# Kernel tuning notes

Measured on AMD Instinct MI355X. Metric: run time of the kernel, lower is better.

## Reference

```python
import jax, jax.numpy as jnp
import numpy as np
import math

B, T, C, H = 4, 4096, 1024, 16
D = C // H

def setup_inputs() -> dict:
    key = jax.random.key(0)
    k1, k2, k3, k4, k5 = jax.random.split(key, 5)
    s = 1.0 / math.sqrt(C)
    return {
        "x": jax.random.normal(k1, (B, T, C), dtype=jnp.float32),
        "W_qkv": jax.random.normal(k2, (C, 3 * C), dtype=jnp.float32) * s,
        "b_qkv": jax.random.normal(k3, (3 * C,), dtype=jnp.float32) * 0.01,
        "W_out": jax.random.normal(k4, (C, C), dtype=jnp.float32) * s,
        "b_out": jax.random.normal(k5, (C,), dtype=jnp.float32) * 0.01,
    }

def reference(x, W_qkv, b_qkv, W_out, b_out):
    qkv = x @ W_qkv + b_qkv                      # (B,T,3C)
    q, k, v = jnp.split(qkv, 3, axis=2)
    q = q.reshape(B, T, H, D)
    k = k.reshape(B, T, H, D)
    v = v.reshape(B, T, H, D)
    # attention over the HEAD axis per (B,T): scores (B,T,H,H)
    att = jnp.einsum('bthd,btgd->bthg', q, k) / math.sqrt(D)
    att = jax.nn.softmax(att, axis=-1)
    out = jnp.einsum('bthg,btgd->bthd', att, v)  # (B,T,H,D)
    out = out.reshape(B, T, C)
    return out @ W_out + b_out
```

## Files before the change

kernel.cpp:

```cpp
#include <hip/hip_runtime.h>
#include <cstdint>
#include <cstddef>

constexpr int Bc = 4;
constexpr int Tc = 4096;
constexpr int Cc = 1024;
constexpr int Hc = 16;
constexpr int Dc = 64;
constexpr int Mc = Bc * Tc;
constexpr int N1c = 3 * Cc;
constexpr int Kc = Cc;
constexpr int KBc = Kc / 32;

typedef __bf16 bf16x8 __attribute__((ext_vector_type(8)));
typedef float  f32x4  __attribute__((ext_vector_type(4)));
typedef __attribute__((address_space(1))) uint32_t gu32;
typedef __attribute__((address_space(3))) uint32_t lu32;

__device__ __forceinline__ float bf2f(unsigned short u) {
    return __uint_as_float(((unsigned)u) << 16);
}
__device__ __forceinline__ unsigned short f2bf(float f) {
    unsigned u = __float_as_uint(f);
    u += 0x7FFF + ((u >> 16) & 1);
    return (unsigned short)(u >> 16);
}

__device__ __forceinline__ void load_lds16(const void* g, void* l) {
    __builtin_amdgcn_global_load_lds((gu32*)(uintptr_t)g, (lu32*)(uintptr_t)l, 16, 0, 0);
}


__global__ void convert_x_packed(const float* __restrict__ x,
                                 unsigned short* __restrict__ Ap) {
    const int w = threadIdx.x >> 6, lane = threadIdx.x & 63;
    const int t = blockIdx.x * 4 + w;
    const int mb = t >> 5, kb = t & 31;
    const int r = lane >> 2, c = lane & 3;
    const float* src = x + (size_t)(mb * 16 + r) * Kc + kb * 32 + c * 8;
    float4 f0 = *(const float4*)src;
    float4 f1 = *(const float4*)(src + 4);
    unsigned short u[8];
    u[0] = f2bf(f0.x); u[1] = f2bf(f0.y); u[2] = f2bf(f0.z); u[3] = f2bf(f0.w);
    u[4] = f2bf(f1.x); u[5] = f2bf(f1.y); u[6] = f2bf(f1.z); u[7] = f2bf(f1.w);
    *(uint4*)(Ap + (size_t)t * 512 + (c * 16 + r) * 8) = *(uint4*)u;
}

__global__ void transpose_convert_packed(const float* __restrict__ W,
                                         unsigned short* __restrict__ Bp,
                                         int K, int N) {
    __shared__ float tile[32][33];
    const int tx = threadIdx.x, ty = threadIdx.y;
    const int n0 = blockIdx.x * 32, k0 = blockIdx.y * 32;
    for (int i = ty; i < 32; i += 8)
        tile[i][tx] = W[(size_t)(k0 + i) * N + n0 + tx];
    __syncthreads();
    const int t = ty * 32 + tx;
    const int h = t >> 7, rr = t & 127, lane = rr >> 1, half = rr & 1;
    const int fq = lane >> 4, fn = lane & 15;
    unsigned short u[4];
    #pragma unroll
    for (int j = 0; j < 4; ++j)
        u[j] = f2bf(tile[fq * 8 + half * 4 + j][h * 16 + fn]);
    size_t tileIdx = (size_t)((n0 >> 4) + h) * (K >> 5) + (k0 >> 5);
    *(uint2*)(Bp + tileIdx * 512 + lane * 8 + half * 4) = *(uint2*)u;
}

template <bool OUT_BF16>
__global__ __launch_bounds__(256, 4) void lds_gemm_kernel(
    const unsigned short* __restrict__ Ap,
    const unsigned short* __restrict__ Bp,
    const float* __restrict__ bias,
    void* __restrict__ Cout,
    int M, int N, int K, int NB) {
    __shared__ unsigned short sA[16 * 512];
    __shared__ unsigned short sB[16 * 512];
    const int KB = K >> 5;
    const int MB = M >> 7;
    const int id   = blockIdx.x;
    const int xcd  = id & 7;
    const int per  = id >> 3;
    const int MSTR = MB >> 3;
    const int byl  = per & 7;
    const int bx   = (per >> 3) % NB;
    const int pass = per / (8 * NB);
    const int by   = xcd * MSTR + pass * 8 + byl;

    const int w    = threadIdx.x >> 6;
    const int lane = threadIdx.x & 63;
    const int m0 = by * 128;
    const int n0 = bx * 128;
    const int wm = (w >> 1) * 64;
    const int wn = (w & 1) * 64;

    const unsigned short* gA[4];
    const unsigned short* gB[4];
    unsigned short* lA[4];
    unsigned short* lB[4];
    #pragma unroll
    for (int i = 0; i < 4; ++i) {
        const int t  = w * 4 + i;
        const int mt = t >> 1, s = t & 1;
        gA[i] = Ap + ((size_t)(by * 8 + mt) * KB + s) * 512 + lane * 8;
        gB[i] = Bp + ((size_t)(bx * 8 + mt) * KB + s) * 512 + lane * 8;
        lA[i] = sA + t * 512;
        lB[i] = sB + t * 512;
    }

    const unsigned short* aP = sA + (wm >> 4) * 2 * 512 + lane * 8;
    const unsigned short* bP = sB + (wn >> 4) * 2 * 512 + lane * 8;

    const f32x4 zero4 = {0.f, 0.f, 0.f, 0.f};
    f32x4 acc[4][4];
    #pragma unroll
    for (int i = 0; i < 4; ++i)
        #pragma unroll
        for (int j = 0; j < 4; ++j) acc[i][j] = zero4;

    const int NIT = K >> 6;
    #pragma unroll 1
    for (int jt = 0; jt < NIT; ++jt) {
        #pragma unroll
        for (int i = 0; i < 4; ++i) {
            load_lds16(gA[i], lA[i]);
            load_lds16(gB[i], lB[i]);
        }
        #pragma unroll
        for (int i = 0; i < 4; ++i) { gA[i] += 1024; gB[i] += 1024; }
        __syncthreads();

        #pragma unroll
        for (int kk = 0; kk < 2; ++kk) {
            bf16x8 af[4], bfr[4];
            #pragma unroll
            for (int mi = 0; mi < 4; ++mi)
                af[mi]  = *(const bf16x8*)(aP + (mi * 2 + kk) * 512);
            #pragma unroll
            for (int ni = 0; ni < 4; ++ni)
                bfr[ni] = *(const bf16x8*)(bP + (ni * 2 + kk) * 512);
            #pragma unroll
            for (int mi = 0; mi < 4; ++mi)
                #pragma unroll
                for (int ni = 0; ni < 4; ++ni)
                    acc[mi][ni] = __builtin_amdgcn_mfma_f32_16x16x32_bf16(
                        af[mi], bfr[ni], acc[mi][ni], 0, 0, 0);
        }
        __syncthreads();
    }

    const int fr = lane & 15;
    const int fq = lane >> 4;
    #pragma unroll
    for (int mi = 0; mi < 4; ++mi) {
        #pragma unroll
        for (int ni = 0; ni < 4; ++ni) {
            int row = m0 + wm + mi * 16 + fq * 4;
            int col = n0 + wn + ni * 16 + fr;
            float bb = bias[col];
            #pragma unroll
            for (int r = 0; r < 4; ++r) {
                float v = acc[mi][ni][r] + bb;
                if (OUT_BF16)
                    ((unsigned short*)Cout)[(size_t)(row + r) * N + col] = f2bf(v);
                else
                    ((float*)Cout)[(size_t)(row + r) * N + col] = v;
            }
        }
    }
}

__global__ __launch_bounds__(256) void attn_mfma_kernel(
    const unsigned short* __restrict__ qkv,
    unsigned short* __restrict__ attP) {
    __shared__ char smem[4 * 3584];
    const int w    = threadIdx.x >> 6;
    const int lane = threadIdx.x & 63;
    const int m    = lane & 15;
    const int q    = lane >> 4;
    const int row  = blockIdx.x * 4 + w;
    unsigned short* sV = (unsigned short*)(smem + w * 3584);
    float*          sP = (float*)(smem + w * 3584 + 2304);

    const unsigned short* src = qkv + (size_t)row * 3072;

    bf16x8 aq0 = *(const bf16x8*)(src + m * 64 + q * 8);
    bf16x8 aq1 = *(const bf16x8*)(src + m * 64 + 32 + q * 8);
    bf16x8 bk0 = *(const bf16x8*)(src + 1024 + m * 64 + q * 8);
    bf16x8 bk1 = *(const bf16x8*)(src + 1024 + m * 64 + 32 + q * 8);

    #pragma unroll
    for (int t = 0; t < 2; ++t) {
        int G = t * 64 + lane;
        int r = G >> 3, p = G & 7;
        *(uint4*)(sV + r * 72 + p * 8) = *(const uint4*)(src + 2048 + G * 8);
    }

    f32x4 s = {0.f, 0.f, 0.f, 0.f};
    s = __builtin_amdgcn_mfma_f32_16x16x32_bf16(aq0, bk0, s, 0, 0, 0);
    s = __builtin_amdgcn_mfma_f32_16x16x32_bf16(aq1, bk1, s, 0, 0, 0);

    #pragma unroll
    for (int r = 0; r < 4; ++r) {
        float t0 = s[r] * 0.125f;
        float mx = t0;
        mx = fmaxf(mx, __shfl_xor(mx, 1));
        mx = fmaxf(mx, __shfl_xor(mx, 2));
        mx = fmaxf(mx, __shfl_xor(mx, 4));
        mx = fmaxf(mx, __shfl_xor(mx, 8));
        float e = __expf(t0 - mx);
        float su = e;
        su += __shfl_xor(su, 1);
        su += __shfl_xor(su, 2);
        su += __shfl_xor(su, 4);
        su += __shfl_xor(su, 8);
        sP[(q * 4 + r) * 20 + m] = e / su;
    }
    __syncthreads();

    const float* pr = sP + m * 20 + (q & 1) * 8;
    float4 pf0 = *(const float4*)(pr);
    float4 pf1 = *(const float4*)(pr + 4);
    const bool act = (q < 2);
    union { unsigned short u[8]; bf16x8 b; } pa;
    pa.u[0] = act ? f2bf(pf0.x) : 0;
    pa.u[1] = act ? f2bf(pf0.y) : 0;
    pa.u[2] = act ? f2bf(pf0.z) : 0;
    pa.u[3] = act ? f2bf(pf0.w) : 0;
    pa.u[4] = act ? f2bf(pf1.x) : 0;
    pa.u[5] = act ? f2bf(pf1.y) : 0;
    pa.u[6] = act ? f2bf(pf1.z) : 0;
    pa.u[7] = act ? f2bf(pf1.w) : 0;

    const unsigned short* vb = sV + (q & 1) * 8 * 72;
    const size_t tileBase = (size_t)(row >> 4) * 32 * 512;
    const int fr_tok = row & 15;
    #pragma unroll
    for (int c4 = 0; c4 < 4; ++c4) {
        union { unsigned short u[8]; bf16x8 b; } vf;
        #pragma unroll
        for (int j = 0; j < 8; ++j) vf.u[j] = vb[j * 72 + c4 * 16 + m];
        f32x4 o = {0.f, 0.f, 0.f, 0.f};
        o = __builtin_amdgcn_mfma_f32_16x16x32_bf16(pa.b, vf.b, o, 0, 0, 0);
        #pragma unroll
        for (int r = 0; r < 4; ++r) {
            int col = (q * 4 + r) * 64 + c4 * 16 + m;
            size_t off = tileBase + (size_t)(col >> 5) * 512
                       + (((col >> 3) & 3) * 16 + fr_tok) * 8 + (col & 7);
            attP[off] = f2bf(o[r]);
        }
    }
}

extern "C" void kernel_launch(void* const* d_in, const int* in_sizes, int n_in,
                              void* d_out, int out_size, void* d_ws, size_t ws_size,
                              hipStream_t stream) {
    const float* x    = (const float*)d_in[0];
    const float* Wqkv = (const float*)d_in[1];
    const float* bqkv = (const float*)d_in[2];
    const float* Wout = (const float*)d_in[3];
    const float* bout = (const float*)d_in[4];
    float* out = (float*)d_out;

    char* ws = (char*)d_ws;
    unsigned short* xp   = (unsigned short*)ws;                 ws += (size_t)Mc * Kc * 2;
    unsigned short* Wqkp = (unsigned short*)ws;                 ws += (size_t)N1c * Kc * 2;
    unsigned short* Wop  = (unsigned short*)ws;                 ws += (size_t)Cc * Kc * 2;
    unsigned short* qkv  = (unsigned short*)ws;
    unsigned short* attP = xp;

    convert_x_packed<<<(Mc / 16) * KBc / 4, 256, 0, stream>>>(x, xp);
    transpose_convert_packed<<<dim3(N1c / 32, Kc / 32), dim3(32, 8), 0, stream>>>(Wqkv, Wqkp, Kc, N1c);
    transpose_convert_packed<<<dim3(Cc / 32, Kc / 32), dim3(32, 8), 0, stream>>>(Wout, Wop, Kc, Cc);
    lds_gemm_kernel<true><<<(N1c / 128) * (Mc / 128), 256, 0, stream>>>(
        xp, Wqkp, bqkv, qkv, Mc, N1c, Kc, N1c / 128);
    attn_mfma_kernel<<<Mc / 4, 256, 0, stream>>>(qkv, attP);
    lds_gemm_kernel<false><<<(Cc / 128) * (Mc / 128), 256, 0, stream>>>(
        attP, Wop, bout, out, Mc, Cc, Kc, Cc / 128);
}
```

Measured before the change: 303.0 us.

## Merge prep kernels, transpose V in QKV epilogue, row-major attention output

Folds the three conversion and transpose launches into one prep kernel dispatched by block id, which cuts launch overhead. The QKV GEMM epilogue now writes V transposed (d-major), so the attention kernel loads V fragments with one 16-byte LDS read instead of eight scalar gathers. The attention output is written row-major with contiguous per-lane stores, and the output GEMM reads A in row-major form through global_load_lds. The trade-off is scattered 2-byte stores for V in the GEMM epilogue and less coalesced A loads in the second GEMM.

```diff
diff --git a/kernel.cpp b/kernel.cpp
--- a/kernel.cpp
+++ b/kernel.cpp
@@ -31,42 +31,50 @@
 }
 
 
-__global__ void convert_x_packed(const float* __restrict__ x,
-                                 unsigned short* __restrict__ Ap) {
-    const int w = threadIdx.x >> 6, lane = threadIdx.x & 63;
-    const int t = blockIdx.x * 4 + w;
-    const int mb = t >> 5, kb = t & 31;
-    const int r = lane >> 2, c = lane & 3;
-    const float* src = x + (size_t)(mb * 16 + r) * Kc + kb * 32 + c * 8;
-    float4 f0 = *(const float4*)src;
-    float4 f1 = *(const float4*)(src + 4);
-    unsigned short u[8];
-    u[0] = f2bf(f0.x); u[1] = f2bf(f0.y); u[2] = f2bf(f0.z); u[3] = f2bf(f0.w);
-    u[4] = f2bf(f1.x); u[5] = f2bf(f1.y); u[6] = f2bf(f1.z); u[7] = f2bf(f1.w);
-    *(uint4*)(Ap + (size_t)t * 512 + (c * 16 + r) * 8) = *(uint4*)u;
-}
-
-__global__ void transpose_convert_packed(const float* __restrict__ W,
-                                         unsigned short* __restrict__ Bp,
-                                         int K, int N) {
+__global__ __launch_bounds__(256) void prep_kernel(
+    const float* __restrict__ x,    unsigned short* __restrict__ Ap,
+    const float* __restrict__ Wqkv, unsigned short* __restrict__ Wqkp,
+    const float* __restrict__ Wout, unsigned short* __restrict__ Wop) {
     __shared__ float tile[32][33];
-    const int tx = threadIdx.x, ty = threadIdx.y;
-    const int n0 = blockIdx.x * 32, k0 = blockIdx.y * 32;
+    const int bid = blockIdx.x;
+    const int tid = threadIdx.x;
+
+    if (bid < 8192) {
+        const int w = tid >> 6, lane = tid & 63;
+        const int t = bid * 4 + w;
+        const int mb = t >> 5, kb = t & 31;
+        const int r = lane >> 2, c = lane & 3;
+        const float* src = x + (size_t)(mb * 16 + r) * Kc + kb * 32 + c * 8;
+        float4 f0 = *(const float4*)src;
+        float4 f1 = *(const float4*)(src + 4);
+        unsigned short u[8];
+        u[0] = f2bf(f0.x); u[1] = f2bf(f0.y); u[2] = f2bf(f0.z); u[3] = f2bf(f0.w);
+        u[4] = f2bf(f1.x); u[5] = f2bf(f1.y); u[6] = f2bf(f1.z); u[7] = f2bf(f1.w);
+        *(uint4*)(Ap + (size_t)t * 512 + (c * 16 + r) * 8) = *(uint4*)u;
+        return;
+    }
+
+    const float* W; unsigned short* Bp; int N; int b2;
+    if (bid < 8192 + 3072) { W = Wqkv; Bp = Wqkp; N = 3072; b2 = bid - 8192; }
+    else                   { W = Wout; Bp = Wop;  N = 1024; b2 = bid - 11264; }
+    const int NT = N >> 5;
+    const int n0 = (b2 % NT) * 32, k0 = (b2 / NT) * 32;
+    const int tx = tid & 31, ty = tid >> 5;
     for (int i = ty; i < 32; i += 8)
         tile[i][tx] = W[(size_t)(k0 + i) * N + n0 + tx];
     __syncthreads();
-    const int t = ty * 32 + tx;
+    const int t = tid;
     const int h = t >> 7, rr = t & 127, lane = rr >> 1, half = rr & 1;
     const int fq = lane >> 4, fn = lane & 15;
     unsigned short u[4];
     #pragma unroll
     for (int j = 0; j < 4; ++j)
         u[j] = f2bf(tile[fq * 8 + half * 4 + j][h * 16 + fn]);
-    size_t tileIdx = (size_t)((n0 >> 4) + h) * (K >> 5) + (k0 >> 5);
+    size_t tileIdx = (size_t)((n0 >> 4) + h) * (Kc >> 5) + (k0 >> 5);
     *(uint2*)(Bp + tileIdx * 512 + lane * 8 + half * 4) = *(uint2*)u;
 }
 
-template <bool OUT_BF16>
+template <bool OUT_BF16, bool VPERM, bool AROW>
 __global__ __launch_bounds__(256, 4) void lds_gemm_kernel(
     const unsigned short* __restrict__ Ap,
     const unsigned short* __restrict__ Bp,
@@ -97,14 +105,20 @@
     const unsigned short* gB[4];
     unsigned short* lA[4];
     unsigned short* lB[4];
-    #pragma unroll
-    for (int i = 0; i < 4; ++i) {
-        const int t  = w * 4 + i;
-        const int mt = t >> 1, s = t & 1;
-        gA[i] = Ap + ((size_t)(by * 8 + mt) * KB + s) * 512 + lane * 8;
-        gB[i] = Bp + ((size_t)(bx * 8 + mt) * KB + s) * 512 + lane * 8;
-        lA[i] = sA + t * 512;
-        lB[i] = sB + t * 512;
+    {
+        const int frl = lane & 15, fql = lane >> 4;
+        #pragma unroll
+        for (int i = 0; i < 4; ++i) {
+            const int t  = w * 4 + i;
+            const int mt = t >> 1, s = t & 1;
+            if (AROW)
+                gA[i] = Ap + ((size_t)((by * 8 + mt) * 16 + frl)) * K + s * 32 + fql * 8;
+            else
+                gA[i] = Ap + ((size_t)(by * 8 + mt) * KB + s) * 512 + lane * 8;
+            gB[i] = Bp + ((size_t)(bx * 8 + mt) * KB + s) * 512 + lane * 8;
+            lA[i] = sA + t * 512;
+            lB[i] = sB + t * 512;
+        }
     }
 
     const unsigned short* aP = sA + (wm >> 4) * 2 * 512 + lane * 8;
@@ -126,7 +140,7 @@
             load_lds16(gB[i], lB[i]);
         }
         #pragma unroll
-        for (int i = 0; i < 4; ++i) { gA[i] += 1024; gB[i] += 1024; }
+        for (int i = 0; i < 4; ++i) { gA[i] += AROW ? 64 : 1024; gB[i] += 1024; }
         __syncthreads();
 
         #pragma unroll
@@ -157,13 +171,18 @@
             int row = m0 + wm + mi * 16 + fq * 4;
             int col = n0 + wn + ni * 16 + fr;
             float bb = bias[col];
+            int scol = col;
+            if (VPERM && col >= 2048) {
+                int c = col - 2048;
+                scol = 2048 + ((c & 63) << 4) + (c >> 6);
+            }
             #pragma unroll
             for (int r = 0; r < 4; ++r) {
                 float v = acc[mi][ni][r] + bb;
                 if (OUT_BF16)
-                    ((unsigned short*)Cout)[(size_t)(row + r) * N + col] = f2bf(v);
+                    ((unsigned short*)Cout)[(size_t)(row + r) * N + scol] = f2bf(v);
                 else
-                    ((float*)Cout)[(size_t)(row + r) * N + col] = v;
+                    ((float*)Cout)[(size_t)(row + r) * N + scol] = v;
             }
         }
     }
@@ -171,15 +190,15 @@
 
 __global__ __launch_bounds__(256) void attn_mfma_kernel(
     const unsigned short* __restrict__ qkv,
-    unsigned short* __restrict__ attP) {
-    __shared__ char smem[4 * 3584];
+    unsigned short* __restrict__ attR) {
+    __shared__ char smem[4 * 4352];
     const int w    = threadIdx.x >> 6;
     const int lane = threadIdx.x & 63;
     const int m    = lane & 15;
     const int q    = lane >> 4;
     const int row  = blockIdx.x * 4 + w;
-    unsigned short* sV = (unsigned short*)(smem + w * 3584);
-    float*          sP = (float*)(smem + w * 3584 + 2304);
+    unsigned short* sVt = (unsigned short*)(smem + w * 4352);
+    float*          sP  = (float*)(smem + w * 4352 + 3072);
 
     const unsigned short* src = qkv + (size_t)row * 3072;
 
@@ -191,8 +210,8 @@
     #pragma unroll
     for (int t = 0; t < 2; ++t) {
         int G = t * 64 + lane;
-        int r = G >> 3, p = G & 7;
-        *(uint4*)(sV + r * 72 + p * 8) = *(const uint4*)(src + 2048 + G * 8);
+        int d = G >> 1, hf = G & 1;
+        *(uint4*)(sVt + d * 24 + hf * 8) = *(const uint4*)(src + 2048 + G * 8);
     }
 
     f32x4 s = {0.f, 0.f, 0.f, 0.f};
@@ -231,22 +250,17 @@
     pa.u[6] = act ? f2bf(pf1.z) : 0;
     pa.u[7] = act ? f2bf(pf1.w) : 0;
 
-    const unsigned short* vb = sV + (q & 1) * 8 * 72;
-    const size_t tileBase = (size_t)(row >> 4) * 32 * 512;
-    const int fr_tok = row & 15;
+    const unsigned short* vrow = sVt + (q & 1) * 8;
+    unsigned short* outp = attR + (size_t)row * 1024;
     #pragma unroll
     for (int c4 = 0; c4 < 4; ++c4) {
-        union { unsigned short u[8]; bf16x8 b; } vf;
-        #pragma unroll
-        for (int j = 0; j < 8; ++j) vf.u[j] = vb[j * 72 + c4 * 16 + m];
+        bf16x8 vf = *(const bf16x8*)(vrow + (c4 * 16 + m) * 24);
         f32x4 o = {0.f, 0.f, 0.f, 0.f};
-        o = __builtin_amdgcn_mfma_f32_16x16x32_bf16(pa.b, vf.b, o, 0, 0, 0);
+        o = __builtin_amdgcn_mfma_f32_16x16x32_bf16(pa.b, vf, o, 0, 0, 0);
         #pragma unroll
         for (int r = 0; r < 4; ++r) {
-            int col = (q * 4 + r) * 64 + c4 * 16 + m;
-            size_t off = tileBase + (size_t)(col >> 5) * 512
-                       + (((col >> 3) & 3) * 16 + fr_tok) * 8 + (col & 7);
-            attP[off] = f2bf(o[r]);
+            int ch = (q * 4 + r) * 64 + c4 * 16 + m;
+            outp[ch] = f2bf(o[r]);
         }
     }
 }
@@ -266,14 +280,12 @@
     unsigned short* Wqkp = (unsigned short*)ws;                 ws += (size_t)N1c * Kc * 2;
     unsigned short* Wop  = (unsigned short*)ws;                 ws += (size_t)Cc * Kc * 2;
     unsigned short* qkv  = (unsigned short*)ws;
-    unsigned short* attP = xp;
-
-    convert_x_packed<<<(Mc / 16) * KBc / 4, 256, 0, stream>>>(x, xp);
-    transpose_convert_packed<<<dim3(N1c / 32, Kc / 32), dim3(32, 8), 0, stream>>>(Wqkv, Wqkp, Kc, N1c);
-    transpose_convert_packed<<<dim3(Cc / 32, Kc / 32), dim3(32, 8), 0, stream>>>(Wout, Wop, Kc, Cc);
-    lds_gemm_kernel<true><<<(N1c / 128) * (Mc / 128), 256, 0, stream>>>(
+    unsigned short* attR = xp;
+
+    prep_kernel<<<8192 + 3072 + 1024, 256, 0, stream>>>(x, xp, Wqkv, Wqkp, Wout, Wop);
+    lds_gemm_kernel<true, true, false><<<(N1c / 128) * (Mc / 128), 256, 0, stream>>>(
         xp, Wqkp, bqkv, qkv, Mc, N1c, Kc, N1c / 128);
-    attn_mfma_kernel<<<Mc / 4, 256, 0, stream>>>(qkv, attP);
-    lds_gemm_kernel<false><<<(Cc / 128) * (Mc / 128), 256, 0, stream>>>(
-        attP, Wop, bout, out, Mc, Cc, Kc, Cc / 128);
-}
+    attn_mfma_kernel<<<Mc / 4, 256, 0, stream>>>(qkv, attR);
+    lds_gemm_kernel<false, false, true><<<(Cc / 128) * (Mc / 128), 256, 0, stream>>>(
+        attR, Wop, bout, out, Mc, Cc, Kc, Cc / 128);
+}
```

New measurement: 349.4 us. 15.3% more time.
